# Performance work log

Hardware: AMD Instinct MI355X
Metric: run time of the kernel (lower is better)

Reference implementation:

```python
import jax, jax.numpy as jnp
import numpy as np

P_DIMS = [512, 256, 128]
K_DIMS = [256, 256, 256]
NT = 65536


def setup_inputs() -> dict:
    key = jax.random.key(0)
    ks = jax.random.split(key, 8 * len(P_DIMS))
    inp = {}
    ki = 0
    for i, (p, k) in enumerate(zip(P_DIMS, K_DIMS)):
        inp[f"x{i}"] = jax.random.normal(ks[ki], (NT, p), jnp.float32); ki += 1
        inp[f"alpha{i}"] = jax.random.normal(ks[ki], (1, k), jnp.float32); ki += 1
        inp[f"beta{i}"] = jax.random.normal(ks[ki], (k, p), jnp.float32) * 0.05; ki += 1
        inp[f"sig{i}"] = jax.random.normal(ks[ki], (1, k), jnp.float32); ki += 1
        inp[f"eta{i}"] = jax.random.normal(ks[ki], (1, k), jnp.float32); ki += 1
        inp[f"gam{i}"] = jax.random.normal(ks[ki], (k, 1), jnp.float32) * 0.03; ki += 1
        inp[f"w{i}"] = jax.random.normal(ks[ki], (k, p), jnp.float32); ki += 1
        inp[f"disc{i}"] = jnp.array([3.0], jnp.float32); ki += 1
    return inp


def _source(x, alpha, beta, sig, eta, gam, w, disc):
    # x: (nt,p); w,beta: (k,p); alpha,sig,eta: (1,k); gam: (k,1); disc: (1,)
    h = eta ** 2                                           # (1,k)
    d2 = (jnp.sum(x * x, axis=1, keepdims=True)
          - 2.0 * (x @ w.T)
          + jnp.sum(w * w, axis=1)[None, :])
    a = jnp.exp(-(gam[:, 0] ** 2)[None, :] * d2)           # (nt,k)
    ah = a * h                                             # a * H
    hx = jnp.sum(ah, axis=1)                               # (nt,)
    mu = x @ beta.T + alpha                                # (nt,k)
    mux = jnp.sum(mu * ah, axis=1) / hx
    sig2x = jnp.sum((sig ** 2) * (ah ** 2), axis=1) / (hx * hx)
    hx_dc = hx * jax.nn.sigmoid(disc[0])
    return mux, sig2x, hx, hx_dc


def reference(x0, alpha0, beta0, sig0, eta0, gam0, w0, disc0,
              x1, alpha1, beta1, sig1, eta1, gam1, w1, disc1,
              x2, alpha2, beta2, sig2, eta2, gam2, w2, disc2):
    srcs = [
        (x0, alpha0, beta0, sig0, eta0, gam0, w0, disc0),
        (x1, alpha1, beta1, sig1, eta1, gam1, w1, disc1),
        (x2, alpha2, beta2, sig2, eta2, gam2, w2, disc2),
    ]
    outs = [_source(*s) for s in srcs]  # fixed small loop over sources
    mux_t = jnp.stack([o[0] for o in outs])     # (S,nt)
    sig2x_t = jnp.stack([o[1] for o in outs])
    hx_t = jnp.stack([o[2] for o in outs])
    hx_dc = jnp.stack([o[3] for o in outs])
    denom = jnp.sum(hx_dc, axis=0)
    mux_comb = jnp.sum(mux_t * hx_dc, axis=0) / denom
    sig2x_comb = jnp.sum(sig2x_t * hx_dc ** 2, axis=0) / (denom ** 2)
    mux_final = jnp.concatenate([mux_t, mux_comb[None]], axis=0)      # (S+1,nt)
    sig2x_final = jnp.concatenate([sig2x_t, sig2x_comb[None]], axis=0)
    hx_final = jnp.concatenate([hx_t, denom[None]], axis=0)
    return (mux_final, sig2x_final, hx_final)
```

## Files before the change

### kernel.cpp

```cpp
#include <hip/hip_runtime.h>
#include <hip/hip_bf16.h>

typedef __attribute__((ext_vector_type(8))) short short8;
typedef __attribute__((ext_vector_type(4))) float f32x4;

#define NT 65536
#define KC 256

__device__ __forceinline__ unsigned short f2bf(float f) {
    union { float f; unsigned int u; } v; v.f = f;
    unsigned int u = v.u;
    unsigned int r = (u + 0x7fffu + ((u >> 16) & 1u)) >> 16;
    return (unsigned short)r;
}

__device__ __forceinline__ unsigned int cvt_pk_bf16(float lo, float hi) {
    unsigned int r;
    asm("v_cvt_pk_bf16_f32 %0, %1, %2" : "=v"(r) : "v"(lo), "v"(hi));
    return r;
}

__global__ void prep_kernel(const float* __restrict__ w, const float* __restrict__ beta,
                            const float* __restrict__ alpha, const float* __restrict__ sig,
                            const float* __restrict__ eta, const float* __restrict__ gam,
                            unsigned short* __restrict__ bc, float* __restrict__ prm, int P) {
    __shared__ float red[2];
    const int n = blockIdx.x;
    const int tid = threadIdx.x;
    const int gidx = n >> 7;
    const int j = n & 127;
    const int k = 64 * gidx + (j & 63);
    const bool isw = (j < 64);
    const float* src = (isw ? w : beta) + (size_t)k * P;
    unsigned short* dst = bc + (size_t)n * P;
    float ss = 0.f;
    for (int c = tid; c < P; c += 128) {
        float f = src[c];
        dst[c] = f2bf(f);
        if (isw) ss += f * f;
    }
#pragma unroll
    for (int m = 1; m < 64; m <<= 1) ss += __shfl_xor(ss, m);
    if ((tid & 63) == 0) red[tid >> 6] = ss;
    __syncthreads();
    if (isw && tid == 0) prm[k] = red[0] + red[1];
    if (n == 0) {
        for (int kk = tid; kk < KC; kk += 128) {
            float g = gam[kk], e = eta[kk];
            prm[KC + kk]     = g * g;
            prm[2 * KC + kk] = e * e;
            prm[3 * KC + kk] = alpha[kk];
            prm[4 * KC + kk] = sig[kk] * sig[kk];
        }
    }
}

__global__ __launch_bounds__(256, 2)
void fused_kernel(const float* __restrict__ x0, const float* __restrict__ x1, const float* __restrict__ x2,
                  const unsigned short* __restrict__ bcAll, const float* __restrict__ prmAll,
                  float* __restrict__ out) {
    __shared__ unsigned short As[2][64 * 32];
    __shared__ unsigned short Bs[2][512 * 32];

    const int bx = blockIdx.x;
    const int s  = bx % 3;
    const int mb = bx / 3;
    const int P  = (s == 0) ? 512 : ((s == 1) ? 256 : 128);
    const int NS = P >> 5;
    const float* x = (s == 0) ? x0 : ((s == 1) ? x1 : x2);
    const unsigned short* Bc = bcAll + ((s == 0) ? 0 : ((s == 1) ? (512 * 512) : (512 * 512 + 512 * 256)));
    const float* prms = prmAll + s * 5 * KC;
    const int row0 = mb * 64;

    const int tid  = threadIdx.x;
    const int lane = tid & 63;
    const int wc   = tid >> 6;
    const int l15 = lane & 15;
    const int l4  = lane >> 4;
    const int fslot = l4 ^ ((l15 >> 1) & 3);

    f32x4 acc[4][8];
#pragma unroll
    for (int rf = 0; rf < 4; rf++)
#pragma unroll
        for (int cf = 0; cf < 8; cf++) acc[rf][cf] = (f32x4){0.f, 0.f, 0.f, 0.f};

    const int arow = tid >> 2;
    const int aseg = tid & 3;
    const int aslot = aseg ^ ((arow >> 1) & 3);
    const float* xrow = x + (size_t)(row0 + arow) * P + aseg * 8;
    float ss = 0.f;

    auto stageB = [&](int nb, int ks) {
#pragma unroll
        for (int i = 0; i < 8; i++) {
            const int u = i * 256 + tid;
            const int r = u >> 2;
            const int sl = (u & 3) ^ ((r >> 1) & 3);
            const unsigned short* src = Bc + (size_t)r * P + ks * 32 + sl * 8;
            unsigned short* dstbase = &Bs[nb][i * 2048 + wc * 512];
            __builtin_amdgcn_global_load_lds((const __attribute__((address_space(1))) void*)src,
                                             (__attribute__((address_space(3))) void*)dstbase, 16, 0, 0);
        }
    };

    stageB(0, 0);
    {
        float4 a0 = *(const float4*)(xrow);
        float4 a1 = *(const float4*)(xrow + 4);
        ss += a0.x*a0.x + a0.y*a0.y + a0.z*a0.z + a0.w*a0.w;
        ss += a1.x*a1.x + a1.y*a1.y + a1.z*a1.z + a1.w*a1.w;
        uint4 pk = { cvt_pk_bf16(a0.x, a0.y), cvt_pk_bf16(a0.z, a0.w),
                     cvt_pk_bf16(a1.x, a1.y), cvt_pk_bf16(a1.z, a1.w) };
        *(uint4*)(&As[0][arow * 32 + aslot * 8]) = pk;
    }
    __syncthreads();

    int buf = 0;
    for (int ks = 0; ks < NS; ks++) {
        const bool more = (ks + 1 < NS);
        float4 a0, a1;
        if (more) {
            stageB(buf ^ 1, ks + 1);
            a0 = *(const float4*)(xrow + (ks + 1) * 32);
            a1 = *(const float4*)(xrow + (ks + 1) * 32 + 4);
        }
        short8 af[4];
#pragma unroll
        for (int rf = 0; rf < 4; rf++)
            af[rf] = *(const short8*)(&As[buf][(16 * rf + l15) * 32 + fslot * 8]);
#pragma unroll
        for (int cf = 0; cf < 8; cf++) {
            const int brow = 128 * wc + 16 * cf + l15;
            const short8 bfv = *(const short8*)(&Bs[buf][brow * 32 + fslot * 8]);
#pragma unroll
            for (int rf = 0; rf < 4; rf++)
                acc[rf][cf] = __builtin_amdgcn_mfma_f32_16x16x32_bf16(af[rf], bfv, acc[rf][cf], 0, 0, 0);
        }
        if (more) {
            ss += a0.x*a0.x + a0.y*a0.y + a0.z*a0.z + a0.w*a0.w;
            ss += a1.x*a1.x + a1.y*a1.y + a1.z*a1.z + a1.w*a1.w;
            uint4 pk = { cvt_pk_bf16(a0.x, a0.y), cvt_pk_bf16(a0.z, a0.w),
                         cvt_pk_bf16(a1.x, a1.y), cvt_pk_bf16(a1.z, a1.w) };
            *(uint4*)(&As[buf ^ 1][arow * 32 + aslot * 8]) = pk;
        }
        __syncthreads();
        buf ^= 1;
    }

    float* xn2 = (float*)(&As[1][0]);
    float sred = ss;
    sred += __shfl_xor(sred, 1);
    sred += __shfl_xor(sred, 2);
    if (aseg == 0) xn2[arow] = sred;
    __syncthreads();

    float xr[4][4];
#pragma unroll
    for (int rf = 0; rf < 4; rf++)
#pragma unroll
        for (int r = 0; r < 4; r++)
            xr[rf][r] = xn2[16 * rf + 4 * l4 + r];

    float hxa[4][4] = {{0}}, mua[4][4] = {{0}}, s2a[4][4] = {{0}};
#pragma unroll
    for (int q = 0; q < 4; q++) {
        const int k = 64 * wc + 16 * q + l15;
        const float wn2v = prms[k];
        const float g2v  = prms[KC + k];
        const float hv   = prms[2 * KC + k];
        const float alv  = prms[3 * KC + k];
        const float s2v  = prms[4 * KC + k];
#pragma unroll
        for (int rf = 0; rf < 4; rf++) {
            const f32x4 aw = acc[rf][q];
            const f32x4 ab = acc[rf][q + 4];
#pragma unroll
            for (int r = 0; r < 4; r++) {
                float d2 = xr[rf][r] - 2.f * aw[r] + wn2v;
                float a  = __expf(-g2v * d2);
                float ah = a * hv;
                hxa[rf][r] += ah;
                mua[rf][r] += (ab[r] + alv) * ah;
                s2a[rf][r] += s2v * ah * ah;
            }
        }
    }

    float (*part)[64][3] = (float (*)[64][3])(&As[0][0]);
#pragma unroll
    for (int rf = 0; rf < 4; rf++) {
#pragma unroll
        for (int r = 0; r < 4; r++) {
            float h = hxa[rf][r], m = mua[rf][r], g = s2a[rf][r];
#pragma unroll
            for (int msk = 1; msk < 16; msk <<= 1) {
                h += __shfl_xor(h, msk);
                m += __shfl_xor(m, msk);
                g += __shfl_xor(g, msk);
            }
            if (l15 == 0) {
                const int row = 16 * rf + 4 * l4 + r;
                part[wc][row][0] = h;
                part[wc][row][1] = m;
                part[wc][row][2] = g;
            }
        }
    }
    __syncthreads();
    if (tid < 64) {
        float h = part[0][tid][0] + part[1][tid][0] + part[2][tid][0] + part[3][tid][0];
        float m = part[0][tid][1] + part[1][tid][1] + part[2][tid][1] + part[3][tid][1];
        float g = part[0][tid][2] + part[1][tid][2] + part[2][tid][2] + part[3][tid][2];
        const int R = row0 + tid;
        out[(size_t)s * NT + R]       = m / h;
        out[(size_t)(4 + s) * NT + R] = g / (h * h);
        out[(size_t)(8 + s) * NT + R] = h;
    }
}

__global__ void combine_kernel(const float* __restrict__ d0, const float* __restrict__ d1,
                               const float* __restrict__ d2, float* out) {
    const int t = blockIdx.x * 256 + threadIdx.x;
    const float sd0 = 1.f / (1.f + __expf(-d0[0]));
    const float sd1 = 1.f / (1.f + __expf(-d1[0]));
    const float sd2 = 1.f / (1.f + __expf(-d2[0]));
    const float hx0 = out[(size_t)8 * NT + t];
    const float hx1 = out[(size_t)9 * NT + t];
    const float hx2 = out[(size_t)10 * NT + t];
    const float c0 = hx0 * sd0, c1 = hx1 * sd1, c2 = hx2 * sd2;
    const float den = c0 + c1 + c2;
    const float muc = out[(size_t)0 * NT + t] * c0 + out[(size_t)1 * NT + t] * c1 + out[(size_t)2 * NT + t] * c2;
    const float sgc = out[(size_t)4 * NT + t] * c0 * c0 + out[(size_t)5 * NT + t] * c1 * c1 + out[(size_t)6 * NT + t] * c2 * c2;
    out[(size_t)3 * NT + t]  = muc / den;
    out[(size_t)7 * NT + t]  = sgc / (den * den);
    out[(size_t)11 * NT + t] = den;
}

extern "C" void kernel_launch(void* const* d_in, const int* in_sizes, int n_in,
                              void* d_out, int out_size, void* d_ws, size_t ws_size,
                              hipStream_t stream) {
    const float* x0 = (const float*)d_in[0];
    const float* x1 = (const float*)d_in[8];
    const float* x2 = (const float*)d_in[16];

    unsigned short* bc = (unsigned short*)d_ws;
    float* prmAll = (float*)((char*)d_ws + 917504);
    float* out = (float*)d_out;

    const int Ps[3] = {512, 256, 128};
    const size_t bcoff[3] = {0, 512 * 512, 512 * 512 + 512 * 256};
    for (int s = 0; s < 3; s++) {
        const float* alpha = (const float*)d_in[8 * s + 1];
        const float* beta  = (const float*)d_in[8 * s + 2];
        const float* sig   = (const float*)d_in[8 * s + 3];
        const float* eta   = (const float*)d_in[8 * s + 4];
        const float* gam   = (const float*)d_in[8 * s + 5];
        const float* w     = (const float*)d_in[8 * s + 6];
        prep_kernel<<<512, 128, 0, stream>>>(w, beta, alpha, sig, eta, gam,
                                             bc + bcoff[s], prmAll + s * 5 * KC, Ps[s]);
    }
    fused_kernel<<<3072, 256, 0, stream>>>(x0, x1, x2, bc, prmAll, out);
    combine_kernel<<<256, 256, 0, stream>>>((const float*)d_in[7], (const float*)d_in[15],
                                            (const float*)d_in[23], out);
}
```

Measured before the change: 155.9 us.

## Hold weight fragments in registers and run persistent per-source kernels splitting K

Replaces the single fused kernel with three templated kernels, one per source. Each block keeps its half of the K columns (w and beta bf16 fragments) resident in registers, loops over 8 row tiles, and double-buffers the whole x tile in LDS while prefetching the next. Partial sums for the two K halves go to workspace and are reduced in the combine kernel, which also does the divisions. This removes the repeated B streaming through LDS per row tile, at the cost of heavy register pressure, three serial launches, and extra workspace traffic.

```diff
diff --git a/kernel.cpp b/kernel.cpp
--- a/kernel.cpp
+++ b/kernel.cpp
@@ -5,7 +5,6 @@
 typedef __attribute__((ext_vector_type(4))) float f32x4;
 
 #define NT 65536
-#define KC 256
 
 __device__ __forceinline__ unsigned short f2bf(float f) {
     union { float f; unsigned int u; } v; v.f = f;
@@ -27,10 +26,10 @@
     __shared__ float red[2];
     const int n = blockIdx.x;
     const int tid = threadIdx.x;
-    const int gidx = n >> 7;
-    const int j = n & 127;
-    const int k = 64 * gidx + (j & 63);
-    const bool isw = (j < 64);
+    const int wb = n >> 5;
+    const int j = n & 31;
+    const bool isw = (j < 16);
+    const int k = wb * 16 + (j & 15);
     const float* src = (isw ? w : beta) + (size_t)k * P;
     unsigned short* dst = bc + (size_t)n * P;
     float ss = 0.f;
@@ -45,193 +44,188 @@
     __syncthreads();
     if (isw && tid == 0) prm[k] = red[0] + red[1];
     if (n == 0) {
-        for (int kk = tid; kk < KC; kk += 128) {
+        for (int kk = tid; kk < 256; kk += 128) {
             float g = gam[kk], e = eta[kk];
-            prm[KC + kk]     = g * g;
-            prm[2 * KC + kk] = e * e;
-            prm[3 * KC + kk] = alpha[kk];
-            prm[4 * KC + kk] = sig[kk] * sig[kk];
-        }
-    }
-}
-
-__global__ __launch_bounds__(256, 2)
-void fused_kernel(const float* __restrict__ x0, const float* __restrict__ x1, const float* __restrict__ x2,
-                  const unsigned short* __restrict__ bcAll, const float* __restrict__ prmAll,
-                  float* __restrict__ out) {
-    __shared__ unsigned short As[2][64 * 32];
-    __shared__ unsigned short Bs[2][512 * 32];
+            prm[256 + kk]  = g * g;
+            prm[512 + kk]  = e * e;
+            prm[768 + kk]  = alpha[kk];
+            prm[1024 + kk] = sig[kk] * sig[kk];
+        }
+    }
+}
+
+template<int P>
+__global__ __launch_bounds__(512, 2)
+void fused_src(const float* __restrict__ x, const unsigned short* __restrict__ Bc,
+               const float* __restrict__ prm, float* __restrict__ pws) {
+    constexpr int KS  = P / 32;
+    constexpr int IST = P / 64;
+    constexpr int WIN = (P == 256) ? 4 : 2;
+    __shared__ unsigned short As[2][64 * P];
+    __shared__ float part[8][64][3];
+    __shared__ float xn2s[2][64];
 
     const int bx = blockIdx.x;
-    const int s  = bx % 3;
-    const int mb = bx / 3;
-    const int P  = (s == 0) ? 512 : ((s == 1) ? 256 : 128);
-    const int NS = P >> 5;
-    const float* x = (s == 0) ? x0 : ((s == 1) ? x1 : x2);
-    const unsigned short* Bc = bcAll + ((s == 0) ? 0 : ((s == 1) ? (512 * 512) : (512 * 512 + 512 * 256)));
-    const float* prms = prmAll + s * 5 * KC;
-    const int row0 = mb * 64;
-
-    const int tid  = threadIdx.x;
-    const int lane = tid & 63;
-    const int wc   = tid >> 6;
-    const int l15 = lane & 15;
-    const int l4  = lane >> 4;
-    const int fslot = l4 ^ ((l15 >> 1) & 3);
-
-    f32x4 acc[4][8];
-#pragma unroll
-    for (int rf = 0; rf < 4; rf++)
-#pragma unroll
-        for (int cf = 0; cf < 8; cf++) acc[rf][cf] = (f32x4){0.f, 0.f, 0.f, 0.f};
-
-    const int arow = tid >> 2;
-    const int aseg = tid & 3;
-    const int aslot = aseg ^ ((arow >> 1) & 3);
-    const float* xrow = x + (size_t)(row0 + arow) * P + aseg * 8;
-    float ss = 0.f;
-
-    auto stageB = [&](int nb, int ks) {
-#pragma unroll
-        for (int i = 0; i < 8; i++) {
-            const int u = i * 256 + tid;
-            const int r = u >> 2;
-            const int sl = (u & 3) ^ ((r >> 1) & 3);
-            const unsigned short* src = Bc + (size_t)r * P + ks * 32 + sl * 8;
-            unsigned short* dstbase = &Bs[nb][i * 2048 + wc * 512];
-            __builtin_amdgcn_global_load_lds((const __attribute__((address_space(1))) void*)src,
-                                             (__attribute__((address_space(3))) void*)dstbase, 16, 0, 0);
-        }
-    };
-
-    stageB(0, 0);
+    const int h  = bx & 1;
+    const int rg = bx >> 1;
+    const int tid = threadIdx.x, lane = tid & 63, wv = tid >> 6;
+    const int l15 = lane & 15, l4 = lane >> 4;
+    const int wb = h * 8 + wv;
+
+    short8 Bf[2][KS];
+#pragma unroll
+    for (int st = 0; st < 2; st++)
+#pragma unroll
+        for (int ks = 0; ks < KS; ks++)
+            Bf[st][ks] = *(const short8*)(Bc + (size_t)(wb * 32 + st * 16 + l15) * P + ks * 32 + l4 * 8);
+
+    const int kb = wb * 16 + 4 * l4;
+    const f32x4 wn2 = *(const f32x4*)(prm + kb);
+    const f32x4 g2  = *(const f32x4*)(prm + 256 + kb);
+    const f32x4 hv  = *(const f32x4*)(prm + 512 + kb);
+    const f32x4 alv = *(const f32x4*)(prm + 768 + kb);
+    const f32x4 s2v = *(const f32x4*)(prm + 1024 + kb);
+
+    float* pw = pws + (size_t)h * 3 * NT;
+
+    const int srow = tid >> 3;
+    const int ssl0 = tid & 7;
+
     {
-        float4 a0 = *(const float4*)(xrow);
-        float4 a1 = *(const float4*)(xrow + 4);
-        ss += a0.x*a0.x + a0.y*a0.y + a0.z*a0.z + a0.w*a0.w;
-        ss += a1.x*a1.x + a1.y*a1.y + a1.z*a1.z + a1.w*a1.w;
-        uint4 pk = { cvt_pk_bf16(a0.x, a0.y), cvt_pk_bf16(a0.z, a0.w),
-                     cvt_pk_bf16(a1.x, a1.y), cvt_pk_bf16(a1.z, a1.w) };
-        *(uint4*)(&As[0][arow * 32 + aslot * 8]) = pk;
-    }
-    __syncthreads();
-
-    int buf = 0;
-    for (int ks = 0; ks < NS; ks++) {
-        const bool more = (ks + 1 < NS);
-        float4 a0, a1;
-        if (more) {
-            stageB(buf ^ 1, ks + 1);
-            a0 = *(const float4*)(xrow + (ks + 1) * 32);
-            a1 = *(const float4*)(xrow + (ks + 1) * 32 + 4);
-        }
-        short8 af[4];
-#pragma unroll
-        for (int rf = 0; rf < 4; rf++)
-            af[rf] = *(const short8*)(&As[buf][(16 * rf + l15) * 32 + fslot * 8]);
-#pragma unroll
-        for (int cf = 0; cf < 8; cf++) {
-            const int brow = 128 * wc + 16 * cf + l15;
-            const short8 bfv = *(const short8*)(&Bs[buf][brow * 32 + fslot * 8]);
-#pragma unroll
-            for (int rf = 0; rf < 4; rf++)
-                acc[rf][cf] = __builtin_amdgcn_mfma_f32_16x16x32_bf16(af[rf], bfv, acc[rf][cf], 0, 0, 0);
-        }
-        if (more) {
-            ss += a0.x*a0.x + a0.y*a0.y + a0.z*a0.z + a0.w*a0.w;
-            ss += a1.x*a1.x + a1.y*a1.y + a1.z*a1.z + a1.w*a1.w;
+        const int row0 = rg * 64;
+        float4 pa[IST], pb[IST];
+#pragma unroll
+        for (int i = 0; i < IST; i++) {
+            const float* gp = x + (size_t)(row0 + srow) * P + (ssl0 + 8 * i) * 8;
+            pa[i] = *(const float4*)(gp);
+            pb[i] = *(const float4*)(gp + 4);
+        }
+        float ssacc = 0.f;
+#pragma unroll
+        for (int i = 0; i < IST; i++) {
+            float4 a0 = pa[i], a1 = pb[i];
+            ssacc += a0.x*a0.x + a0.y*a0.y + a0.z*a0.z + a0.w*a0.w
+                   + a1.x*a1.x + a1.y*a1.y + a1.z*a1.z + a1.w*a1.w;
             uint4 pk = { cvt_pk_bf16(a0.x, a0.y), cvt_pk_bf16(a0.z, a0.w),
                          cvt_pk_bf16(a1.x, a1.y), cvt_pk_bf16(a1.z, a1.w) };
-            *(uint4*)(&As[buf ^ 1][arow * 32 + aslot * 8]) = pk;
+            const int slot = ssl0 + 8 * i;
+            *(uint4*)(&As[0][srow * P + ((slot ^ (srow & 7)) << 3)]) = pk;
+        }
+        ssacc += __shfl_xor(ssacc, 1);
+        ssacc += __shfl_xor(ssacc, 2);
+        ssacc += __shfl_xor(ssacc, 4);
+        if (ssl0 == 0) xn2s[0][srow] = ssacc;
+    }
+    __syncthreads();
+
+    int buf = 0;
+    for (int tt = 0; tt < 8; tt++) {
+        const int tile = rg + 128 * tt;
+        const int row0 = tile * 64;
+        const bool more = (tt < 7);
+        const int nrow0 = (tile + 128) * 64;
+
+        f32x4 acc[2][4];
+#pragma unroll
+        for (int st = 0; st < 2; st++)
+#pragma unroll
+            for (int rf = 0; rf < 4; rf++) acc[st][rf] = (f32x4){0.f, 0.f, 0.f, 0.f};
+
+        float4 gfa[WIN], gfb[WIN];
+        float ssacc = 0.f;
+
+#pragma unroll
+        for (int ks = 0; ks < KS; ks++) {
+            if (more && ks >= WIN && (ks - WIN) < IST) {
+                const int i = ks - WIN;
+                float4 a0 = gfa[i % WIN], a1 = gfb[i % WIN];
+                ssacc += a0.x*a0.x + a0.y*a0.y + a0.z*a0.z + a0.w*a0.w
+                       + a1.x*a1.x + a1.y*a1.y + a1.z*a1.z + a1.w*a1.w;
+                uint4 pk = { cvt_pk_bf16(a0.x, a0.y), cvt_pk_bf16(a0.z, a0.w),
+                             cvt_pk_bf16(a1.x, a1.y), cvt_pk_bf16(a1.z, a1.w) };
+                const int slot = ssl0 + 8 * i;
+                *(uint4*)(&As[buf ^ 1][srow * P + ((slot ^ (srow & 7)) << 3)]) = pk;
+            }
+            if (more && ks < IST) {
+                const float* gp = x + (size_t)(nrow0 + srow) * P + (ssl0 + 8 * ks) * 8;
+                gfa[ks % WIN] = *(const float4*)(gp);
+                gfb[ks % WIN] = *(const float4*)(gp + 4);
+            }
+            short8 af[4];
+#pragma unroll
+            for (int rf = 0; rf < 4; rf++) {
+                const int row = 16 * rf + l15;
+                af[rf] = *(const short8*)(&As[buf][row * P + (((ks * 4 + l4) ^ (row & 7)) << 3)]);
+            }
+#pragma unroll
+            for (int rf = 0; rf < 4; rf++) {
+                acc[0][rf] = __builtin_amdgcn_mfma_f32_16x16x32_bf16(Bf[0][ks], af[rf], acc[0][rf], 0, 0, 0);
+                acc[1][rf] = __builtin_amdgcn_mfma_f32_16x16x32_bf16(Bf[1][ks], af[rf], acc[1][rf], 0, 0, 0);
+            }
+        }
+
+        if (more) {
+            ssacc += __shfl_xor(ssacc, 1);
+            ssacc += __shfl_xor(ssacc, 2);
+            ssacc += __shfl_xor(ssacc, 4);
+            if (ssl0 == 0) xn2s[buf ^ 1][srow] = ssacc;
+        }
+
+#pragma unroll
+        for (int rf = 0; rf < 4; rf++) {
+            const int row = 16 * rf + l15;
+            const float xv = xn2s[buf][row];
+            float hs = 0.f, ms = 0.f, gs = 0.f;
+#pragma unroll
+            for (int j = 0; j < 4; j++) {
+                float d2 = xv - 2.f * acc[0][rf][j] + wn2[j];
+                float a  = __expf(-g2[j] * d2);
+                float ah = a * hv[j];
+                hs += ah;
+                ms += (acc[1][rf][j] + alv[j]) * ah;
+                gs += s2v[j] * ah * ah;
+            }
+            hs += __shfl_xor(hs, 16); hs += __shfl_xor(hs, 32);
+            ms += __shfl_xor(ms, 16); ms += __shfl_xor(ms, 32);
+            gs += __shfl_xor(gs, 16); gs += __shfl_xor(gs, 32);
+            if (l4 == 0) { part[wv][row][0] = hs; part[wv][row][1] = ms; part[wv][row][2] = gs; }
+        }
+        __syncthreads();
+        if (tid < 192) {
+            const int v = tid >> 6, r = tid & 63;
+            float sum = 0.f;
+#pragma unroll
+            for (int w8 = 0; w8 < 8; w8++) sum += part[w8][r][v];
+            pw[(size_t)v * NT + row0 + r] = sum;
         }
         __syncthreads();
         buf ^= 1;
     }
-
-    float* xn2 = (float*)(&As[1][0]);
-    float sred = ss;
-    sred += __shfl_xor(sred, 1);
-    sred += __shfl_xor(sred, 2);
-    if (aseg == 0) xn2[arow] = sred;
-    __syncthreads();
-
-    float xr[4][4];
-#pragma unroll
-    for (int rf = 0; rf < 4; rf++)
-#pragma unroll
-        for (int r = 0; r < 4; r++)
-            xr[rf][r] = xn2[16 * rf + 4 * l4 + r];
-
-    float hxa[4][4] = {{0}}, mua[4][4] = {{0}}, s2a[4][4] = {{0}};
-#pragma unroll
-    for (int q = 0; q < 4; q++) {
-        const int k = 64 * wc + 16 * q + l15;
-        const float wn2v = prms[k];
-        const float g2v  = prms[KC + k];
-        const float hv   = prms[2 * KC + k];
-        const float alv  = prms[3 * KC + k];
-        const float s2v  = prms[4 * KC + k];
-#pragma unroll
-        for (int rf = 0; rf < 4; rf++) {
-            const f32x4 aw = acc[rf][q];
-            const f32x4 ab = acc[rf][q + 4];
-#pragma unroll
-            for (int r = 0; r < 4; r++) {
-                float d2 = xr[rf][r] - 2.f * aw[r] + wn2v;
-                float a  = __expf(-g2v * d2);
-                float ah = a * hv;
-                hxa[rf][r] += ah;
-                mua[rf][r] += (ab[r] + alv) * ah;
-                s2a[rf][r] += s2v * ah * ah;
-            }
-        }
-    }
-
-    float (*part)[64][3] = (float (*)[64][3])(&As[0][0]);
-#pragma unroll
-    for (int rf = 0; rf < 4; rf++) {
-#pragma unroll
-        for (int r = 0; r < 4; r++) {
-            float h = hxa[rf][r], m = mua[rf][r], g = s2a[rf][r];
-#pragma unroll
-            for (int msk = 1; msk < 16; msk <<= 1) {
-                h += __shfl_xor(h, msk);
-                m += __shfl_xor(m, msk);
-                g += __shfl_xor(g, msk);
-            }
-            if (l15 == 0) {
-                const int row = 16 * rf + 4 * l4 + r;
-                part[wc][row][0] = h;
-                part[wc][row][1] = m;
-                part[wc][row][2] = g;
-            }
-        }
-    }
-    __syncthreads();
-    if (tid < 64) {
-        float h = part[0][tid][0] + part[1][tid][0] + part[2][tid][0] + part[3][tid][0];
-        float m = part[0][tid][1] + part[1][tid][1] + part[2][tid][1] + part[3][tid][1];
-        float g = part[0][tid][2] + part[1][tid][2] + part[2][tid][2] + part[3][tid][2];
-        const int R = row0 + tid;
-        out[(size_t)s * NT + R]       = m / h;
-        out[(size_t)(4 + s) * NT + R] = g / (h * h);
-        out[(size_t)(8 + s) * NT + R] = h;
-    }
-}
-
-__global__ void combine_kernel(const float* __restrict__ d0, const float* __restrict__ d1,
-                               const float* __restrict__ d2, float* out) {
+}
+
+__global__ void combine_kernel(const float* __restrict__ pws,
+                               const float* __restrict__ d0, const float* __restrict__ d1,
+                               const float* __restrict__ d2, float* __restrict__ out) {
     const int t = blockIdx.x * 256 + threadIdx.x;
+    float mux[3], s2x[3], hx[3];
+#pragma unroll
+    for (int s = 0; s < 3; s++) {
+        const float* b = pws + (size_t)s * 6 * NT;
+        const float hh = b[t] + b[(size_t)3 * NT + t];
+        const float mm = b[(size_t)1 * NT + t] + b[(size_t)4 * NT + t];
+        const float gg = b[(size_t)2 * NT + t] + b[(size_t)5 * NT + t];
+        mux[s] = mm / hh; s2x[s] = gg / (hh * hh); hx[s] = hh;
+        out[(size_t)s * NT + t]       = mux[s];
+        out[(size_t)(4 + s) * NT + t] = s2x[s];
+        out[(size_t)(8 + s) * NT + t] = hh;
+    }
     const float sd0 = 1.f / (1.f + __expf(-d0[0]));
     const float sd1 = 1.f / (1.f + __expf(-d1[0]));
     const float sd2 = 1.f / (1.f + __expf(-d2[0]));
-    const float hx0 = out[(size_t)8 * NT + t];
-    const float hx1 = out[(size_t)9 * NT + t];
-    const float hx2 = out[(size_t)10 * NT + t];
-    const float c0 = hx0 * sd0, c1 = hx1 * sd1, c2 = hx2 * sd2;
+    const float c0 = hx[0] * sd0, c1 = hx[1] * sd1, c2 = hx[2] * sd2;
     const float den = c0 + c1 + c2;
-    const float muc = out[(size_t)0 * NT + t] * c0 + out[(size_t)1 * NT + t] * c1 + out[(size_t)2 * NT + t] * c2;
-    const float sgc = out[(size_t)4 * NT + t] * c0 * c0 + out[(size_t)5 * NT + t] * c1 * c1 + out[(size_t)6 * NT + t] * c2 * c2;
+    const float muc = mux[0] * c0 + mux[1] * c1 + mux[2] * c2;
+    const float sgc = s2x[0] * c0 * c0 + s2x[1] * c1 * c1 + s2x[2] * c2 * c2;
     out[(size_t)3 * NT + t]  = muc / den;
     out[(size_t)7 * NT + t]  = sgc / (den * den);
     out[(size_t)11 * NT + t] = den;
@@ -246,21 +240,20 @@
 
     unsigned short* bc = (unsigned short*)d_ws;
     float* prmAll = (float*)((char*)d_ws + 917504);
+    float* pws    = (float*)((char*)d_ws + 917504 + 15360);
     float* out = (float*)d_out;
 
     const int Ps[3] = {512, 256, 128};
     const size_t bcoff[3] = {0, 512 * 512, 512 * 512 + 512 * 256};
     for (int s = 0; s < 3; s++) {
-        const float* alpha = (const float*)d_in[8 * s + 1];
-        const float* beta  = (const float*)d_in[8 * s + 2];
-        const float* sig   = (const float*)d_in[8 * s + 3];
-        const float* eta   = (const float*)d_in[8 * s + 4];
-        const float* gam   = (const float*)d_in[8 * s + 5];
-        const float* w     = (const float*)d_in[8 * s + 6];
-        prep_kernel<<<512, 128, 0, stream>>>(w, beta, alpha, sig, eta, gam,
-                                             bc + bcoff[s], prmAll + s * 5 * KC, Ps[s]);
-    }
-    fused_kernel<<<3072, 256, 0, stream>>>(x0, x1, x2, bc, prmAll, out);
-    combine_kernel<<<256, 256, 0, stream>>>((const float*)d_in[7], (const float*)d_in[15],
+        prep_kernel<<<512, 128, 0, stream>>>((const float*)d_in[8 * s + 6], (const float*)d_in[8 * s + 2],
+                                             (const float*)d_in[8 * s + 1], (const float*)d_in[8 * s + 3],
+                                             (const float*)d_in[8 * s + 4], (const float*)d_in[8 * s + 5],
+                                             bc + bcoff[s], prmAll + s * 1280, Ps[s]);
+    }
+    fused_src<512><<<256, 512, 0, stream>>>(x0, bc + bcoff[0], prmAll,          pws);
+    fused_src<256><<<256, 512, 0, stream>>>(x1, bc + bcoff[1], prmAll + 1280,   pws + (size_t)6 * NT);
+    fused_src<128><<<256, 512, 0, stream>>>(x2, bc + bcoff[2], prmAll + 2560,   pws + (size_t)12 * NT);
+    combine_kernel<<<256, 256, 0, stream>>>(pws, (const float*)d_in[7], (const float*)d_in[15],
                                             (const float*)d_in[23], out);
 }
```

Measured after the change: 133.9 us. -14.1%, faster.
